# Kernel tuning notes

Hardware: AMD Instinct MI355X
Metric: run time of the kernel (lower is better)

The kernel has to match this reference:

```python
import jax, jax.numpy as jnp
import numpy as np

SEQ, BATCH, IN, H, HFC, OUT, NLAYERS = 1024, 64, 512, 1024, 512, 1, 2


def setup_inputs() -> dict:
    key = jax.random.key(0)
    ks = jax.random.split(key, 16)
    s_in = 1.0 / np.sqrt(H)  # torch RNN init scale: U(-1/sqrt(hidden), 1/sqrt(hidden))
    u = lambda k, shape: jax.random.uniform(k, shape, jnp.float32, -s_in, s_in)
    return {
        "x": jax.random.normal(ks[0], (SEQ, BATCH, IN), jnp.float32),
        "hidden": jnp.zeros((NLAYERS, BATCH, H), jnp.float32),
        # RNN layer 0
        "W_ih0": u(ks[1], (H, IN)),
        "W_hh0": u(ks[2], (H, H)),
        "b_ih0": u(ks[3], (H,)),
        "b_hh0": u(ks[4], (H,)),
        # RNN layer 1
        "W_ih1": u(ks[5], (H, H)),
        "W_hh1": u(ks[6], (H, H)),
        "b_ih1": u(ks[7], (H,)),
        "b_hh1": u(ks[8], (H,)),
        # FC head
        "W1": jax.random.normal(ks[9], (HFC, H), jnp.float32) / np.sqrt(H),
        "b1": jnp.zeros((HFC,), jnp.float32),
        "W2": jax.random.normal(ks[10], (OUT, HFC), jnp.float32) / np.sqrt(HFC),
        "b2": jnp.zeros((OUT,), jnp.float32),
    }


def _rnn_layer(inp, h0, W_ih, W_hh, b_ih, b_hh):
    # inp: (seq, batch, d_in); precompute input projection once (big GEMM)
    xW = jnp.einsum("sbi,hi->sbh", inp, W_ih) + b_ih + b_hh  # (seq, batch, H)

    def step(h, xw):
        h_new = jnp.tanh(xw + h @ W_hh.T)
        return h_new, h_new

    _, outs = jax.lax.scan(step, h0, xW)
    return outs  # (seq, batch, H)


def reference(x, hidden, W_ih0, W_hh0, b_ih0, b_hh0,
              W_ih1, W_hh1, b_ih1, b_hh1, W1, b1, W2, b2):
    r0 = _rnn_layer(x, hidden[0], W_ih0, W_hh0, b_ih0, b_hh0)
    r1 = _rnn_layer(r0, hidden[1], W_ih1, W_hh1, b_ih1, b_hh1)
    # Faithful to source: mean over dim=1, which (batch_first=False) is the batch dim
    pooled = jnp.mean(r1, axis=1)  # (seq, H)
    h1 = jax.nn.relu(pooled @ W1.T + b1)  # dropout is identity in eval mode
    out = jax.nn.sigmoid(h1 @ W2.T + b2)  # (seq, OUT)
    return out
```

## Files before the change

### kernel.cpp

```cpp
#include <hip/hip_runtime.h>

typedef unsigned int uint;
typedef unsigned short ushort;
typedef unsigned long long u64;
typedef __attribute__((ext_vector_type(8))) short s16x8;
typedef __attribute__((ext_vector_type(4))) float f32x4;
typedef __attribute__((ext_vector_type(4))) uint u32x4;

#define SEQ 1024
#define BATCH 64
#define INDIM 512
#define HID 1024

#define OFF_BUF   0ull
#define SZ_BUF    (65536ull * 1024ull * 2ull)
#define OFF_W0B   (OFF_BUF + SZ_BUF)
#define OFF_WH0B  (OFF_W0B  + 1048576ull)
#define OFF_W1B   (OFF_WH0B + 2097152ull)
#define OFF_WH1B  (OFF_W1B  + 2097152ull)
#define OFF_HINIT (OFF_WH1B + 2097152ull)
#define OFF_HDB1  (OFF_HINIT + 262144ull)
#define OFF_FLG   (OFF_HDB1 + 262144ull)
#define OFF_RING  (OFF_FLG + 131072ull)
#define OFF_PPART (OFF_RING + 4194304ull)
#define WS_NEEDED (OFF_PPART + 16777216ull)

__device__ __forceinline__ ushort f2bf(float f) {
    uint u = __float_as_uint(f);
    uint r = (u + 0x7fffu + ((u >> 16) & 1u)) >> 16;
    return (ushort)r;
}
__device__ __forceinline__ float bf2f(ushort h) {
    return __uint_as_float(((uint)h) << 16);
}

__device__ __forceinline__ void st16wt(void* p, uint v) {
    asm volatile("global_store_short %0, %1, off sc0 sc1"
                 :: "v"((u64)p), "v"(v) : "memory");
}
__device__ __forceinline__ void stf32wt(float* p, float v) {
    asm volatile("global_store_dword %0, %1, off sc0 sc1"
                 :: "v"((u64)p), "v"(v) : "memory");
}

__device__ __forceinline__ void poll_all(const uint* fp, uint tgt) {
    for (;;) {
        uint v = __hip_atomic_load(fp, __ATOMIC_RELAXED, __HIP_MEMORY_SCOPE_AGENT);
        if (__all(v >= tgt)) break;
        __builtin_amdgcn_s_sleep(1);
    }
}

__global__ void k_prep(const float* Wih0, const float* Whh0, const float* Wih1,
                       const float* Whh1, const float* hid, char* ws) {
    ushort* w0  = (ushort*)(ws + OFF_W0B);
    ushort* wh0 = (ushort*)(ws + OFF_WH0B);
    ushort* w1  = (ushort*)(ws + OFF_W1B);
    ushort* wh1 = (ushort*)(ws + OFF_WH1B);
    ushort* hi  = (ushort*)(ws + OFF_HINIT);
    uint*   flg = (uint*)(ws + OFF_FLG);
    const long long total = 524288 + 3 * 1048576 + 131072 + 32768;
    for (long long i = (long long)blockIdx.x * 256 + threadIdx.x; i < total;
         i += (long long)gridDim.x * 256) {
        long long j = i;
        if (j < 524288)  { w0[j]  = f2bf(Wih0[j]); continue; }  j -= 524288;
        if (j < 1048576) { wh0[j] = f2bf(Whh0[j]); continue; }  j -= 1048576;
        if (j < 1048576) { w1[j]  = f2bf(Wih1[j]); continue; }  j -= 1048576;
        if (j < 1048576) { wh1[j] = f2bf(Whh1[j]); continue; }  j -= 1048576;
        if (j < 131072)  { hi[j]  = f2bf(hid[j]);  continue; }  j -= 131072;
        flg[j] = 0u;
    }
}

__launch_bounds__(256)
__global__ void k_proj0(const float* __restrict__ x, const float* __restrict__ bih,
                        const float* __restrict__ bhh, char* ws) {
    const ushort* W = (const ushort*)(ws + OFF_W0B);
    ushort* cbuf = (ushort*)(ws + OFF_BUF);
    int bx = blockIdx.x;
    int mtile = bx >> 2, ntile = bx & 3;
    int tid = threadIdx.x, w = tid >> 6, l = tid & 63;
    int lr = l & 15, lq = l >> 4;
    int arow = mtile * 64 + w * 16 + lr;

    f32x4 acc[16];
#pragma unroll
    for (int i = 0; i < 16; i++) acc[i] = (f32x4){0.f, 0.f, 0.f, 0.f};

    for (int kc = 0; kc < 16; kc++) {
        int k0 = kc * 32 + lq * 8;
        const f32x4* ap = (const f32x4*)(x + (long long)arow * 512 + k0);
        f32x4 a0 = ap[0], a1 = ap[1];
        s16x8 a;
        a[0] = (short)f2bf(a0[0]); a[1] = (short)f2bf(a0[1]);
        a[2] = (short)f2bf(a0[2]); a[3] = (short)f2bf(a0[3]);
        a[4] = (short)f2bf(a1[0]); a[5] = (short)f2bf(a1[1]);
        a[6] = (short)f2bf(a1[2]); a[7] = (short)f2bf(a1[3]);
#pragma unroll
        for (int nf = 0; nf < 16; nf++) {
            int col = ntile * 256 + nf * 16 + lr;
            s16x8 b = *(const s16x8*)(W + (long long)col * 512 + k0);
            acc[nf] = __builtin_amdgcn_mfma_f32_16x16x32_bf16(a, b, acc[nf], 0, 0, 0);
        }
    }
#pragma unroll
    for (int nf = 0; nf < 16; nf++) {
        int col = ntile * 256 + nf * 16 + lr;
        float bb = bih[col] + bhh[col];
#pragma unroll
        for (int j = 0; j < 4; j++) {
            int row = mtile * 64 + w * 16 + lq * 4 + j;
            cbuf[(long long)row * 1024 + col] = f2bf(acc[nf][j] + bb);
        }
    }
}

__launch_bounds__(256, 1)
__global__ void k_recf(const ushort* __restrict__ wh0p, const ushort* __restrict__ wh1p,
                       const ushort* __restrict__ wxp,
                       ushort* __restrict__ cbuf, ushort* __restrict__ hdb1,
                       const ushort* __restrict__ hinitb, uint* __restrict__ flg,
                       float* __restrict__ ring, float* __restrict__ ppart,
                       const float* __restrict__ bih1, const float* __restrict__ bhh1) {
    int wgid = blockIdx.x;
    int x = wgid & 7, hi = wgid >> 3;
    int role, g, s;
    if (x < 4) { g = x; if (hi < 8) { role = 0; s = hi; } else { role = 2; s = hi - 8; } }
    else       { role = 1; g = x - 4; s = hi; }

    int tid = threadIdx.x;
    int l = tid & 63, wv = tid >> 6, lr = l & 15, lq = l >> 4;

    uint* f0g = flg + (g * 8) * 32;
    uint* f1g = flg + 1024 + (g * 8) * 32;
    uint* fcg = flg + 2048 + (g * 16) * 32;

    __shared__ __align__(16) char lds[32768];

    int colA = (role == 1) ? (s * 64 + wv * 16 + lr) : (s * 128 + wv * 16 + lr);
    int colB = (role == 1) ? colA : (s * 128 + 64 + wv * 16 + lr);
    const ushort* Wb = (role == 0) ? wh0p : (role == 1) ? wxp : wh1p;

    s16x8 wgtA[32], wgtB[32];
#pragma unroll
    for (int kc = 0; kc < 32; kc++)
        wgtA[kc] = *(const s16x8*)(Wb + (long long)colA * 1024 + kc * 32 + lq * 8);
#pragma unroll
    for (int kc = 0; kc < 32; kc++) asm volatile("" : "+v"(wgtA[kc]));
    if (role != 1) {
#pragma unroll
        for (int kc = 0; kc < 32; kc++)
            wgtB[kc] = *(const s16x8*)(Wb + (long long)colB * 1024 + kc * 32 + lq * 8);
#pragma unroll
        for (int kc = 0; kc < 32; kc++) asm volatile("" : "+v"(wgtB[kc]));
    }

    if (role == 1) {
        float bb = bih1[colA] + bhh1[colA];
        uint* myslot = fcg + s * 32;
        for (int k = 0; k < 128; k++) {
            if (tid < 64) {
                const uint* fp; uint tgt;
                int sl = l & 15;
                if (sl < 8) { fp = f0g + sl * 32; tgt = (uint)(8 * k + 8); }
                else        { fp = f1g + (sl - 8) * 32; tgt = (k >= 2) ? (uint)(8 * k - 8) : 0u; }
                poll_all(fp, tgt);
                if (l == 0)
                    (void)__hip_atomic_load(f0g, __ATOMIC_ACQUIRE, __HIP_MEMORY_SCOPE_AGENT);
            }
            __syncthreads();
            for (int tt = 0; tt < 8; tt++) {
                int t = 8 * k + tt;
                const char* src = (const char*)(cbuf + (t * 64 + g * 16) * 1024);
                u32x4 v[8];
#pragma unroll
                for (int i = 0; i < 8; i++)
                    v[i] = *(const u32x4*)(src + tid * 16 + i * 4096);
                __syncthreads();
#pragma unroll
                for (int i = 0; i < 8; i++) {
                    int off = tid * 16 + i * 4096;
                    int row = off >> 11;
                    int sw = (off & 2047) ^ ((row & 7) << 4);
                    *(u32x4*)(lds + row * 2048 + sw) = v[i];
                }
                __syncthreads();
                f32x4 a0c = (f32x4){0.f,0.f,0.f,0.f}, a1c = (f32x4){0.f,0.f,0.f,0.f};
#pragma unroll
                for (int kc = 0; kc < 32; kc += 2) {
                    int b0 = (kc * 64 + lq * 16) ^ ((lr & 7) << 4);
                    int b1 = ((kc + 1) * 64 + lq * 16) ^ ((lr & 7) << 4);
                    s16x8 fA = *(const s16x8*)(lds + lr * 2048 + b0);
                    s16x8 fB = *(const s16x8*)(lds + lr * 2048 + b1);
                    a0c = __builtin_amdgcn_mfma_f32_16x16x32_bf16(fA, wgtA[kc], a0c, 0, 0, 0);
                    a1c = __builtin_amdgcn_mfma_f32_16x16x32_bf16(fB, wgtA[kc + 1], a1c, 0, 0, 0);
                }
                float* rd = ring + (long long)((g * 16 + s) * 16 + (t & 15)) * 1024
                          + (wv * 16 + lr);
#pragma unroll
                for (int j = 0; j < 4; j++)
                    stf32wt(rd + (lq * 4 + j) * 64, a0c[j] + a1c[j] + bb);
            }
            __syncthreads();
            if (tid == 0)
                __hip_atomic_store(myslot, (uint)(8 * k + 8), __ATOMIC_RELEASE,
                                   __HIP_MEMORY_SCOPE_AGENT);
        }
        return;
    }

    uint* myslot = ((role == 0) ? f0g : f1g) + s * 32;
    const ushort* hinit = hinitb + (role == 2 ? 65536 : 0) + g * 16 * 1024;

    for (int t = 0; t < 1024; t++) {
        int cbase = (t * 64 + g * 16) * 1024;

        ushort cfA[4], cfB[4];
        if (role == 0) {
#pragma unroll
            for (int j = 0; j < 4; j++) {
                cfA[j] = cbuf[cbase + (lq * 4 + j) * 1024 + colA];
                cfB[j] = cbuf[cbase + (lq * 4 + j) * 1024 + colB];
            }
        }

        if (tid < 64) {
            if (role == 0) {
                poll_all(f0g + (l & 7) * 32, (uint)t);
            } else {
                const uint* fp; uint tgt;
                int sl = l & 15;
                if (sl < 8) { fp = f1g + sl * 32; tgt = (uint)t; }
                else if (sl < 10) { fp = fcg + (2 * s + (sl - 8)) * 32; tgt = (uint)(t + 1); }
                else { fp = f1g; tgt = (uint)t; }
                poll_all(fp, tgt);
            }
            if (l == 0)
                (void)__hip_atomic_load(f0g, __ATOMIC_ACQUIRE, __HIP_MEMORY_SCOPE_AGENT);
        }
        __syncthreads();

        float c1A[4], c1B[4];
        if (role == 2) {
            const float* rA = ring + (long long)((g * 16 + 2 * s) * 16 + (t & 15)) * 1024
                            + (wv * 16 + lr);
            const float* rB = ring + (long long)((g * 16 + 2 * s + 1) * 16 + (t & 15)) * 1024
                            + (wv * 16 + lr);
#pragma unroll
            for (int j = 0; j < 4; j++) {
                c1A[j] = rA[(lq * 4 + j) * 64];
                c1B[j] = rB[(lq * 4 + j) * 64];
            }
        }

        const char* src;
        if (role == 0)
            src = (const char*)((t == 0) ? hinit
                                         : (cbuf + ((t - 1) * 64 + g * 16) * 1024));
        else
            src = (const char*)((t == 0) ? hinit
                                         : (hdb1 + ((t - 1) & 1) * 65536 + g * 16 * 1024));
#pragma unroll
        for (int i = 0; i < 8; i++) {
            int off = tid * 16 + i * 4096;
            u32x4 v = *(const u32x4*)(src + off);
            int row = off >> 11;
            int sw = (off & 2047) ^ ((row & 7) << 4);
            *(u32x4*)(lds + row * 2048 + sw) = v;
        }
        __syncthreads();

        f32x4 aA0 = (f32x4){0.f,0.f,0.f,0.f}, aA1 = (f32x4){0.f,0.f,0.f,0.f};
        f32x4 aB0 = (f32x4){0.f,0.f,0.f,0.f}, aB1 = (f32x4){0.f,0.f,0.f,0.f};
#pragma unroll
        for (int kc = 0; kc < 32; kc += 2) {
            int b0 = (kc * 64 + lq * 16) ^ ((lr & 7) << 4);
            int b1 = ((kc + 1) * 64 + lq * 16) ^ ((lr & 7) << 4);
            s16x8 h0 = *(const s16x8*)(lds + lr * 2048 + b0);
            s16x8 h1 = *(const s16x8*)(lds + lr * 2048 + b1);
            aA0 = __builtin_amdgcn_mfma_f32_16x16x32_bf16(h0, wgtA[kc], aA0, 0, 0, 0);
            aB0 = __builtin_amdgcn_mfma_f32_16x16x32_bf16(h0, wgtB[kc], aB0, 0, 0, 0);
            aA1 = __builtin_amdgcn_mfma_f32_16x16x32_bf16(h1, wgtA[kc + 1], aA1, 0, 0, 0);
            aB1 = __builtin_amdgcn_mfma_f32_16x16x32_bf16(h1, wgtB[kc + 1], aB1, 0, 0, 0);
        }

        float hnA[4], hnB[4];
#pragma unroll
        for (int j = 0; j < 4; j++) {
            float zA = aA0[j] + aA1[j] + (role == 0 ? bf2f(cfA[j]) : c1A[j]);
            float zB = aB0[j] + aB1[j] + (role == 0 ? bf2f(cfB[j]) : c1B[j]);
            zA = fminf(fmaxf(zA, -15.f), 15.f);
            zB = fminf(fmaxf(zB, -15.f), 15.f);
            float eA = __expf(2.f * zA), eB = __expf(2.f * zB);
            hnA[j] = (eA - 1.f) / (eA + 1.f);
            hnB[j] = (eB - 1.f) / (eB + 1.f);
        }

        if (role == 0) {
#pragma unroll
            for (int j = 0; j < 4; j++) {
                st16wt(cbuf + cbase + (lq * 4 + j) * 1024 + colA, (uint)f2bf(hnA[j]));
                st16wt(cbuf + cbase + (lq * 4 + j) * 1024 + colB, (uint)f2bf(hnB[j]));
            }
        } else {
            ushort* hdst = hdb1 + (t & 1) * 65536 + g * 16 * 1024;
#pragma unroll
            for (int j = 0; j < 4; j++) {
                st16wt(hdst + (lq * 4 + j) * 1024 + colA, (uint)f2bf(hnA[j]));
                st16wt(hdst + (lq * 4 + j) * 1024 + colB, (uint)f2bf(hnB[j]));
            }
            float sA = hnA[0] + hnA[1] + hnA[2] + hnA[3];
            float sB = hnB[0] + hnB[1] + hnB[2] + hnB[3];
            sA += __shfl_xor(sA, 16); sA += __shfl_xor(sA, 32);
            sB += __shfl_xor(sB, 16); sB += __shfl_xor(sB, 32);
            if (l < 16) {
                stf32wt(&ppart[(g * 1024 + t) * 1024 + colA], sA);
                stf32wt(&ppart[(g * 1024 + t) * 1024 + colB], sB);
            }
        }

        __syncthreads();
        if (tid == 0)
            __hip_atomic_store(myslot, (uint)(t + 1), __ATOMIC_RELEASE,
                               __HIP_MEMORY_SCOPE_AGENT);
    }
}

__launch_bounds__(256)
__global__ void k_head(const float* __restrict__ W1, const float* __restrict__ b1,
                       const float* __restrict__ W2, const float* __restrict__ b2,
                       char* ws, float* __restrict__ out) {
    const float* pp = (const float*)(ws + OFF_PPART);
    int bx = blockIdx.x;
    int t0 = bx * 8;
    int tid = threadIdx.x;

    __shared__ float pl[8][1024];
    __shared__ float red[256][8];

    for (int i = tid; i < 8192; i += 256) {
        int tt = i >> 10, k = i & 1023;
        int base = (t0 + tt) * 1024 + k;
        float s = pp[base] + pp[1048576 + base] + pp[2097152 + base] + pp[3145728 + base];
        pl[tt][k] = s * (1.f / 64.f);
    }
    __syncthreads();

    float po[8];
#pragma unroll
    for (int tt = 0; tt < 8; tt++) po[tt] = 0.f;

    for (int jj = 0; jj < 2; jj++) {
        int j = tid + jj * 256;
        float accv[8];
        float bias = b1[j];
#pragma unroll
        for (int tt = 0; tt < 8; tt++) accv[tt] = bias;
        const float* wr = W1 + (long long)j * 1024;
        for (int k = 0; k < 1024; k += 8) {
            f32x4 wa = *(const f32x4*)(wr + k);
            f32x4 wb = *(const f32x4*)(wr + k + 4);
#pragma unroll
            for (int tt = 0; tt < 8; tt++) {
                accv[tt] += pl[tt][k] * wa[0] + pl[tt][k + 1] * wa[1] +
                            pl[tt][k + 2] * wa[2] + pl[tt][k + 3] * wa[3] +
                            pl[tt][k + 4] * wb[0] + pl[tt][k + 5] * wb[1] +
                            pl[tt][k + 6] * wb[2] + pl[tt][k + 7] * wb[3];
            }
        }
        float w2 = W2[j];
#pragma unroll
        for (int tt = 0; tt < 8; tt++) po[tt] += fmaxf(accv[tt], 0.f) * w2;
    }

#pragma unroll
    for (int tt = 0; tt < 8; tt++) red[tid][tt] = po[tt];
    __syncthreads();
    for (int st = 128; st >= 1; st >>= 1) {
        if (tid < st) {
#pragma unroll
            for (int tt = 0; tt < 8; tt++) red[tid][tt] += red[tid + st][tt];
        }
        __syncthreads();
    }
    if (tid < 8) out[t0 + tid] = 1.f / (1.f + __expf(-(red[0][tid] + b2[0])));
}

extern "C" void kernel_launch(void* const* d_in, const int* in_sizes, int n_in,
                              void* d_out, int out_size, void* d_ws, size_t ws_size,
                              hipStream_t stream) {
    const float* x    = (const float*)d_in[0];
    const float* hid  = (const float*)d_in[1];
    const float* Wih0 = (const float*)d_in[2];
    const float* Whh0 = (const float*)d_in[3];
    const float* bih0 = (const float*)d_in[4];
    const float* bhh0 = (const float*)d_in[5];
    const float* Wih1 = (const float*)d_in[6];
    const float* Whh1 = (const float*)d_in[7];
    const float* bih1 = (const float*)d_in[8];
    const float* bhh1 = (const float*)d_in[9];
    const float* W1   = (const float*)d_in[10];
    const float* b1   = (const float*)d_in[11];
    const float* W2   = (const float*)d_in[12];
    const float* b2   = (const float*)d_in[13];
    char* ws = (char*)d_ws;
    float* out = (float*)d_out;

    hipLaunchKernelGGL(k_prep, dim3(1024), dim3(256), 0, stream,
                       Wih0, Whh0, Wih1, Whh1, hid, ws);
    hipLaunchKernelGGL(k_proj0, dim3(4096), dim3(256), 0, stream, x, bih0, bhh0, ws);
    hipLaunchKernelGGL(k_recf, dim3(128), dim3(256), 0, stream,
                       (const ushort*)(ws + OFF_WH0B), (const ushort*)(ws + OFF_WH1B),
                       (const ushort*)(ws + OFF_W1B),
                       (ushort*)(ws + OFF_BUF), (ushort*)(ws + OFF_HDB1),
                       (const ushort*)(ws + OFF_HINIT), (uint*)(ws + OFF_FLG),
                       (float*)(ws + OFF_RING), (float*)(ws + OFF_PPART),
                       bih1, bhh1);
    hipLaunchKernelGGL(k_head, dim3(128), dim3(256), 0, stream, W1, b1, W2, b2, ws, out);
}
```

Baseline: 6.574 ms.

## Repartition recurrent kernel into two batch groups of 32 rows across 48 workgroups

The persistent recurrent kernel now splits the batch into 2 groups of 32 rows instead of 4 groups of 16, and each workgroup runs two M-tiles per step. The layer-1 input-projection role now covers 128 columns like the recurrent roles, so the grid drops from 128 to 48 workgroups. The aim is fewer workgroups and fewer flags to synchronise, more MFMA work per weight register load, and a cheaper head reduction over 2 partial sums instead of 4. In exchange each step does twice the per-workgroup compute and LDS traffic, with a 64KB LDS buffer, which may lengthen the serial critical path of each timestep.

```diff
diff --git a/kernel.cpp b/kernel.cpp
--- a/kernel.cpp
+++ b/kernel.cpp
@@ -23,7 +23,7 @@
 #define OFF_FLG   (OFF_HDB1 + 262144ull)
 #define OFF_RING  (OFF_FLG + 131072ull)
 #define OFF_PPART (OFF_RING + 4194304ull)
-#define WS_NEEDED (OFF_PPART + 16777216ull)
+#define WS_NEEDED (OFF_PPART + 8388608ull)
 
 __device__ __forceinline__ ushort f2bf(float f) {
     uint u = __float_as_uint(f);
@@ -123,22 +123,22 @@
                        float* __restrict__ ring, float* __restrict__ ppart,
                        const float* __restrict__ bih1, const float* __restrict__ bhh1) {
     int wgid = blockIdx.x;
-    int x = wgid & 7, hi = wgid >> 3;
-    int role, g, s;
-    if (x < 4) { g = x; if (hi < 8) { role = 0; s = hi; } else { role = 2; s = hi - 8; } }
-    else       { role = 1; g = x - 4; s = hi; }
+    int x = wgid & 7, h = wgid >> 3;
+    int g = x >> 2;
+    int idx = (x & 3) * 6 + h;
+    int role = idx >> 3, s = idx & 7;
 
     int tid = threadIdx.x;
     int l = tid & 63, wv = tid >> 6, lr = l & 15, lq = l >> 4;
 
     uint* f0g = flg + (g * 8) * 32;
     uint* f1g = flg + 1024 + (g * 8) * 32;
-    uint* fcg = flg + 2048 + (g * 16) * 32;
-
-    __shared__ __align__(16) char lds[32768];
-
-    int colA = (role == 1) ? (s * 64 + wv * 16 + lr) : (s * 128 + wv * 16 + lr);
-    int colB = (role == 1) ? colA : (s * 128 + 64 + wv * 16 + lr);
+    uint* fcg = flg + 2048 + (g * 8) * 32;
+
+    __shared__ __align__(16) char lds[65536];
+
+    int colA = s * 128 + wv * 16 + lr;
+    int colB = colA + 64;
     const ushort* Wb = (role == 0) ? wh0p : (role == 1) ? wxp : wh1p;
 
     s16x8 wgtA[32], wgtB[32];
@@ -147,16 +147,34 @@
         wgtA[kc] = *(const s16x8*)(Wb + (long long)colA * 1024 + kc * 32 + lq * 8);
 #pragma unroll
     for (int kc = 0; kc < 32; kc++) asm volatile("" : "+v"(wgtA[kc]));
-    if (role != 1) {
-#pragma unroll
-        for (int kc = 0; kc < 32; kc++)
-            wgtB[kc] = *(const s16x8*)(Wb + (long long)colB * 1024 + kc * 32 + lq * 8);
-#pragma unroll
-        for (int kc = 0; kc < 32; kc++) asm volatile("" : "+v"(wgtB[kc]));
+#pragma unroll
+    for (int kc = 0; kc < 32; kc++)
+        wgtB[kc] = *(const s16x8*)(Wb + (long long)colB * 1024 + kc * 32 + lq * 8);
+#pragma unroll
+    for (int kc = 0; kc < 32; kc++) asm volatile("" : "+v"(wgtB[kc]));
+
+#define STWR(i, val) { int off = tid * 16 + (i) * 4096; int row = off >> 11;        \
+                       int sw = (off & 2047) ^ ((row & 7) << 4);                    \
+                       *(u32x4*)(lds + row * 2048 + sw) = (val); }
+#define GEMM32(accA, accB)                                                          \
+    _Pragma("unroll")                                                               \
+    for (int kc = 0; kc < 32; kc += 2) {                                            \
+        int b0 = (kc * 64 + lq * 16) ^ ((lr & 7) << 4);                             \
+        int b1 = ((kc + 1) * 64 + lq * 16) ^ ((lr & 7) << 4);                       \
+        _Pragma("unroll")                                                           \
+        for (int m = 0; m < 2; m++) {                                               \
+            s16x8 h0 = *(const s16x8*)(lds + (m * 16 + lr) * 2048 + b0);            \
+            s16x8 h1 = *(const s16x8*)(lds + (m * 16 + lr) * 2048 + b1);            \
+            accA[m][0] = __builtin_amdgcn_mfma_f32_16x16x32_bf16(h0, wgtA[kc], accA[m][0], 0, 0, 0); \
+            accB[m][0] = __builtin_amdgcn_mfma_f32_16x16x32_bf16(h0, wgtB[kc], accB[m][0], 0, 0, 0); \
+            accA[m][1] = __builtin_amdgcn_mfma_f32_16x16x32_bf16(h1, wgtA[kc + 1], accA[m][1], 0, 0, 0); \
+            accB[m][1] = __builtin_amdgcn_mfma_f32_16x16x32_bf16(h1, wgtB[kc + 1], accB[m][1], 0, 0, 0); \
+        }                                                                           \
     }
 
     if (role == 1) {
-        float bb = bih1[colA] + bhh1[colA];
+        float bbA = bih1[colA] + bhh1[colA];
+        float bbB = bih1[colB] + bhh1[colB];
         uint* myslot = fcg + s * 32;
         for (int k = 0; k < 128; k++) {
             if (tid < 64) {
@@ -171,35 +189,35 @@
             __syncthreads();
             for (int tt = 0; tt < 8; tt++) {
                 int t = 8 * k + tt;
-                const char* src = (const char*)(cbuf + (t * 64 + g * 16) * 1024);
-                u32x4 v[8];
-#pragma unroll
-                for (int i = 0; i < 8; i++)
+                const char* src = (const char*)(cbuf + (t * 64 + g * 32) * 1024);
+                u32x4 v[16];
+#pragma unroll
+                for (int i = 0; i < 16; i++)
                     v[i] = *(const u32x4*)(src + tid * 16 + i * 4096);
                 __syncthreads();
 #pragma unroll
-                for (int i = 0; i < 8; i++) {
-                    int off = tid * 16 + i * 4096;
-                    int row = off >> 11;
-                    int sw = (off & 2047) ^ ((row & 7) << 4);
-                    *(u32x4*)(lds + row * 2048 + sw) = v[i];
-                }
+                for (int i = 0; i < 16; i++) STWR(i, v[i])
                 __syncthreads();
-                f32x4 a0c = (f32x4){0.f,0.f,0.f,0.f}, a1c = (f32x4){0.f,0.f,0.f,0.f};
-#pragma unroll
-                for (int kc = 0; kc < 32; kc += 2) {
-                    int b0 = (kc * 64 + lq * 16) ^ ((lr & 7) << 4);
-                    int b1 = ((kc + 1) * 64 + lq * 16) ^ ((lr & 7) << 4);
-                    s16x8 fA = *(const s16x8*)(lds + lr * 2048 + b0);
-                    s16x8 fB = *(const s16x8*)(lds + lr * 2048 + b1);
-                    a0c = __builtin_amdgcn_mfma_f32_16x16x32_bf16(fA, wgtA[kc], a0c, 0, 0, 0);
-                    a1c = __builtin_amdgcn_mfma_f32_16x16x32_bf16(fB, wgtA[kc + 1], a1c, 0, 0, 0);
-                }
-                float* rd = ring + (long long)((g * 16 + s) * 16 + (t & 15)) * 1024
+                f32x4 accA[2][2], accB[2][2];
+#pragma unroll
+                for (int m = 0; m < 2; m++)
+#pragma unroll
+                    for (int u = 0; u < 2; u++) {
+                        accA[m][u] = (f32x4){0.f, 0.f, 0.f, 0.f};
+                        accB[m][u] = (f32x4){0.f, 0.f, 0.f, 0.f};
+                    }
+                GEMM32(accA, accB)
+                float* rd = ring + (long long)((g * 8 + s) * 16 + (t & 15)) * 4096
                           + (wv * 16 + lr);
 #pragma unroll
-                for (int j = 0; j < 4; j++)
-                    stf32wt(rd + (lq * 4 + j) * 64, a0c[j] + a1c[j] + bb);
+                for (int m = 0; m < 2; m++)
+#pragma unroll
+                    for (int j = 0; j < 4; j++) {
+                        stf32wt(rd + (m * 16 + lq * 4 + j) * 128,
+                                accA[m][0][j] + accA[m][1][j] + bbA);
+                        stf32wt(rd + (m * 16 + lq * 4 + j) * 128 + 64,
+                                accB[m][0][j] + accB[m][1][j] + bbB);
+                    }
             }
             __syncthreads();
             if (tid == 0)
@@ -210,18 +228,20 @@
     }
 
     uint* myslot = ((role == 0) ? f0g : f1g) + s * 32;
-    const ushort* hinit = hinitb + (role == 2 ? 65536 : 0) + g * 16 * 1024;
+    const ushort* hinit = hinitb + (role == 2 ? 65536 : 0) + g * 32 * 1024;
 
     for (int t = 0; t < 1024; t++) {
-        int cbase = (t * 64 + g * 16) * 1024;
-
-        ushort cfA[4], cfB[4];
+        int cbase = (t * 64 + g * 32) * 1024;
+
+        ushort cfA[2][4], cfB[2][4];
         if (role == 0) {
 #pragma unroll
-            for (int j = 0; j < 4; j++) {
-                cfA[j] = cbuf[cbase + (lq * 4 + j) * 1024 + colA];
-                cfB[j] = cbuf[cbase + (lq * 4 + j) * 1024 + colB];
-            }
+            for (int m = 0; m < 2; m++)
+#pragma unroll
+                for (int j = 0; j < 4; j++) {
+                    cfA[m][j] = cbuf[cbase + (m * 16 + lq * 4 + j) * 1024 + colA];
+                    cfB[m][j] = cbuf[cbase + (m * 16 + lq * 4 + j) * 1024 + colB];
+                }
         }
 
         if (tid < 64) {
@@ -229,10 +249,9 @@
                 poll_all(f0g + (l & 7) * 32, (uint)t);
             } else {
                 const uint* fp; uint tgt;
-                int sl = l & 15;
-                if (sl < 8) { fp = f1g + sl * 32; tgt = (uint)t; }
-                else if (sl < 10) { fp = fcg + (2 * s + (sl - 8)) * 32; tgt = (uint)(t + 1); }
-                else { fp = f1g; tgt = (uint)t; }
+                if (l < 8)       { fp = f1g + l * 32; tgt = (uint)t; }
+                else if (l == 8) { fp = fcg + s * 32; tgt = (uint)(t + 1); }
+                else             { fp = f1g; tgt = (uint)t; }
                 poll_all(fp, tgt);
             }
             if (l == 0)
@@ -240,77 +259,84 @@
         }
         __syncthreads();
 
-        float c1A[4], c1B[4];
+        float c1A[2][4], c1B[2][4];
         if (role == 2) {
-            const float* rA = ring + (long long)((g * 16 + 2 * s) * 16 + (t & 15)) * 1024
+            const float* rs = ring + (long long)((g * 8 + s) * 16 + (t & 15)) * 4096
                             + (wv * 16 + lr);
-            const float* rB = ring + (long long)((g * 16 + 2 * s + 1) * 16 + (t & 15)) * 1024
-                            + (wv * 16 + lr);
-#pragma unroll
-            for (int j = 0; j < 4; j++) {
-                c1A[j] = rA[(lq * 4 + j) * 64];
-                c1B[j] = rB[(lq * 4 + j) * 64];
-            }
+#pragma unroll
+            for (int m = 0; m < 2; m++)
+#pragma unroll
+                for (int j = 0; j < 4; j++) {
+                    c1A[m][j] = rs[(m * 16 + lq * 4 + j) * 128];
+                    c1B[m][j] = rs[(m * 16 + lq * 4 + j) * 128 + 64];
+                }
         }
 
         const char* src;
         if (role == 0)
             src = (const char*)((t == 0) ? hinit
-                                         : (cbuf + ((t - 1) * 64 + g * 16) * 1024));
+                                         : (cbuf + ((t - 1) * 64 + g * 32) * 1024));
         else
             src = (const char*)((t == 0) ? hinit
-                                         : (hdb1 + ((t - 1) & 1) * 65536 + g * 16 * 1024));
-#pragma unroll
-        for (int i = 0; i < 8; i++) {
-            int off = tid * 16 + i * 4096;
-            u32x4 v = *(const u32x4*)(src + off);
-            int row = off >> 11;
-            int sw = (off & 2047) ^ ((row & 7) << 4);
-            *(u32x4*)(lds + row * 2048 + sw) = v;
+                                         : (hdb1 + ((t - 1) & 1) * 65536 + g * 32 * 1024));
+#pragma unroll
+        for (int i = 0; i < 16; i++) {
+            u32x4 v = *(const u32x4*)(src + tid * 16 + i * 4096);
+            STWR(i, v)
         }
         __syncthreads();
 
-        f32x4 aA0 = (f32x4){0.f,0.f,0.f,0.f}, aA1 = (f32x4){0.f,0.f,0.f,0.f};
-        f32x4 aB0 = (f32x4){0.f,0.f,0.f,0.f}, aB1 = (f32x4){0.f,0.f,0.f,0.f};
-#pragma unroll
-        for (int kc = 0; kc < 32; kc += 2) {
-            int b0 = (kc * 64 + lq * 16) ^ ((lr & 7) << 4);
-            int b1 = ((kc + 1) * 64 + lq * 16) ^ ((lr & 7) << 4);
-            s16x8 h0 = *(const s16x8*)(lds + lr * 2048 + b0);
-            s16x8 h1 = *(const s16x8*)(lds + lr * 2048 + b1);
-            aA0 = __builtin_amdgcn_mfma_f32_16x16x32_bf16(h0, wgtA[kc], aA0, 0, 0, 0);
-            aB0 = __builtin_amdgcn_mfma_f32_16x16x32_bf16(h0, wgtB[kc], aB0, 0, 0, 0);
-            aA1 = __builtin_amdgcn_mfma_f32_16x16x32_bf16(h1, wgtA[kc + 1], aA1, 0, 0, 0);
-            aB1 = __builtin_amdgcn_mfma_f32_16x16x32_bf16(h1, wgtB[kc + 1], aB1, 0, 0, 0);
-        }
-
-        float hnA[4], hnB[4];
-#pragma unroll
-        for (int j = 0; j < 4; j++) {
-            float zA = aA0[j] + aA1[j] + (role == 0 ? bf2f(cfA[j]) : c1A[j]);
-            float zB = aB0[j] + aB1[j] + (role == 0 ? bf2f(cfB[j]) : c1B[j]);
-            zA = fminf(fmaxf(zA, -15.f), 15.f);
-            zB = fminf(fmaxf(zB, -15.f), 15.f);
-            float eA = __expf(2.f * zA), eB = __expf(2.f * zB);
-            hnA[j] = (eA - 1.f) / (eA + 1.f);
-            hnB[j] = (eB - 1.f) / (eB + 1.f);
-        }
+        f32x4 accA[2][2], accB[2][2];
+#pragma unroll
+        for (int m = 0; m < 2; m++)
+#pragma unroll
+            for (int u = 0; u < 2; u++) {
+                accA[m][u] = (f32x4){0.f, 0.f, 0.f, 0.f};
+                accB[m][u] = (f32x4){0.f, 0.f, 0.f, 0.f};
+            }
+        GEMM32(accA, accB)
+
+        float hnA[2][4], hnB[2][4];
+#pragma unroll
+        for (int m = 0; m < 2; m++)
+#pragma unroll
+            for (int j = 0; j < 4; j++) {
+                float zA = accA[m][0][j] + accA[m][1][j]
+                         + (role == 0 ? bf2f(cfA[m][j]) : c1A[m][j]);
+                float zB = accB[m][0][j] + accB[m][1][j]
+                         + (role == 0 ? bf2f(cfB[m][j]) : c1B[m][j]);
+                zA = fminf(fmaxf(zA, -15.f), 15.f);
+                zB = fminf(fmaxf(zB, -15.f), 15.f);
+                float eA = __expf(2.f * zA), eB = __expf(2.f * zB);
+                hnA[m][j] = (eA - 1.f) / (eA + 1.f);
+                hnB[m][j] = (eB - 1.f) / (eB + 1.f);
+            }
 
         if (role == 0) {
 #pragma unroll
-            for (int j = 0; j < 4; j++) {
-                st16wt(cbuf + cbase + (lq * 4 + j) * 1024 + colA, (uint)f2bf(hnA[j]));
-                st16wt(cbuf + cbase + (lq * 4 + j) * 1024 + colB, (uint)f2bf(hnB[j]));
-            }
+            for (int m = 0; m < 2; m++)
+#pragma unroll
+                for (int j = 0; j < 4; j++) {
+                    st16wt(cbuf + cbase + (m * 16 + lq * 4 + j) * 1024 + colA,
+                           (uint)f2bf(hnA[m][j]));
+                    st16wt(cbuf + cbase + (m * 16 + lq * 4 + j) * 1024 + colB,
+                           (uint)f2bf(hnB[m][j]));
+                }
         } else {
-            ushort* hdst = hdb1 + (t & 1) * 65536 + g * 16 * 1024;
-#pragma unroll
-            for (int j = 0; j < 4; j++) {
-                st16wt(hdst + (lq * 4 + j) * 1024 + colA, (uint)f2bf(hnA[j]));
-                st16wt(hdst + (lq * 4 + j) * 1024 + colB, (uint)f2bf(hnB[j]));
-            }
-            float sA = hnA[0] + hnA[1] + hnA[2] + hnA[3];
-            float sB = hnB[0] + hnB[1] + hnB[2] + hnB[3];
+            ushort* hdst = hdb1 + (t & 1) * 65536 + g * 32 * 1024;
+#pragma unroll
+            for (int m = 0; m < 2; m++)
+#pragma unroll
+                for (int j = 0; j < 4; j++) {
+                    st16wt(hdst + (m * 16 + lq * 4 + j) * 1024 + colA,
+                           (uint)f2bf(hnA[m][j]));
+                    st16wt(hdst + (m * 16 + lq * 4 + j) * 1024 + colB,
+                           (uint)f2bf(hnB[m][j]));
+                }
+            float sA = hnA[0][0] + hnA[0][1] + hnA[0][2] + hnA[0][3]
+                     + hnA[1][0] + hnA[1][1] + hnA[1][2] + hnA[1][3];
+            float sB = hnB[0][0] + hnB[0][1] + hnB[0][2] + hnB[0][3]
+                     + hnB[1][0] + hnB[1][1] + hnB[1][2] + hnB[1][3];
             sA += __shfl_xor(sA, 16); sA += __shfl_xor(sA, 32);
             sB += __shfl_xor(sB, 16); sB += __shfl_xor(sB, 32);
             if (l < 16) {
@@ -324,6 +350,8 @@
             __hip_atomic_store(myslot, (uint)(t + 1), __ATOMIC_RELEASE,
                                __HIP_MEMORY_SCOPE_AGENT);
     }
+#undef GEMM32
+#undef STWR
 }
 
 __launch_bounds__(256)
@@ -341,7 +369,7 @@
     for (int i = tid; i < 8192; i += 256) {
         int tt = i >> 10, k = i & 1023;
         int base = (t0 + tt) * 1024 + k;
-        float s = pp[base] + pp[1048576 + base] + pp[2097152 + base] + pp[3145728 + base];
+        float s = pp[base] + pp[1048576 + base];
         pl[tt][k] = s * (1.f / 64.f);
     }
     __syncthreads();
@@ -409,7 +437,7 @@
     hipLaunchKernelGGL(k_prep, dim3(1024), dim3(256), 0, stream,
                        Wih0, Whh0, Wih1, Whh1, hid, ws);
     hipLaunchKernelGGL(k_proj0, dim3(4096), dim3(256), 0, stream, x, bih0, bhh0, ws);
-    hipLaunchKernelGGL(k_recf, dim3(128), dim3(256), 0, stream,
+    hipLaunchKernelGGL(k_recf, dim3(48), dim3(256), 0, stream,
                        (const ushort*)(ws + OFF_WH0B), (const ushort*)(ws + OFF_WH1B),
                        (const ushort*)(ws + OFF_W1B),
                        (ushort*)(ws + OFF_BUF), (ushort*)(ws + OFF_HDB1),
```

New measurement: 9.938 ms. 51.2% more time.

## Fuse layer-1 input projection into layer-1 recurrence workgroups, drop ring buffer

Applied to the files above, without the earlier changes.

Removes the separate role that computed layer-1 input projections in 8-step chunks into a float ring buffer. Each layer-1 workgroup now owns 64 columns and holds both W_hh1 and W_ih1 slices in registers, computing h@W_hh and x@W_ih per step from two LDS tiles. This cuts the extra flag handshake and ring round-trip through global memory and reduces the grid from 128 to 96 workgroups. The cost is twice the MFMA work and staging per step on the layer-1 critical path, and a shorter lookahead for layer 1 behind layer 0.

```diff
diff --git a/kernel.cpp b/kernel.cpp
--- a/kernel.cpp
+++ b/kernel.cpp
@@ -21,8 +21,7 @@
 #define OFF_HINIT (OFF_WH1B + 2097152ull)
 #define OFF_HDB1  (OFF_HINIT + 262144ull)
 #define OFF_FLG   (OFF_HDB1 + 262144ull)
-#define OFF_RING  (OFF_FLG + 131072ull)
-#define OFF_PPART (OFF_RING + 4194304ull)
+#define OFF_PPART (OFF_FLG + 131072ull)
 #define WS_NEEDED (OFF_PPART + 16777216ull)
 
 __device__ __forceinline__ ushort f2bf(float f) {
@@ -120,210 +119,193 @@
                        const ushort* __restrict__ wxp,
                        ushort* __restrict__ cbuf, ushort* __restrict__ hdb1,
                        const ushort* __restrict__ hinitb, uint* __restrict__ flg,
-                       float* __restrict__ ring, float* __restrict__ ppart,
+                       float* __restrict__ ppart,
                        const float* __restrict__ bih1, const float* __restrict__ bhh1) {
     int wgid = blockIdx.x;
-    int x = wgid & 7, hi = wgid >> 3;
-    int role, g, s;
-    if (x < 4) { g = x; if (hi < 8) { role = 0; s = hi; } else { role = 2; s = hi - 8; } }
-    else       { role = 1; g = x - 4; s = hi; }
+    int g = wgid & 3;
+    int r = wgid >> 2;
+    int role = (r < 8) ? 0 : 1;
+    int s = (r < 8) ? r : (r - 8);
 
     int tid = threadIdx.x;
     int l = tid & 63, wv = tid >> 6, lr = l & 15, lq = l >> 4;
 
     uint* f0g = flg + (g * 8) * 32;
-    uint* f1g = flg + 1024 + (g * 8) * 32;
-    uint* fcg = flg + 2048 + (g * 16) * 32;
-
-    __shared__ __align__(16) char lds[32768];
-
-    int colA = (role == 1) ? (s * 64 + wv * 16 + lr) : (s * 128 + wv * 16 + lr);
-    int colB = (role == 1) ? colA : (s * 128 + 64 + wv * 16 + lr);
-    const ushort* Wb = (role == 0) ? wh0p : (role == 1) ? wxp : wh1p;
-
-    s16x8 wgtA[32], wgtB[32];
-#pragma unroll
-    for (int kc = 0; kc < 32; kc++)
-        wgtA[kc] = *(const s16x8*)(Wb + (long long)colA * 1024 + kc * 32 + lq * 8);
-#pragma unroll
-    for (int kc = 0; kc < 32; kc++) asm volatile("" : "+v"(wgtA[kc]));
-    if (role != 1) {
+    uint* f1g = flg + 1024 + (g * 16) * 32;
+
+    __shared__ __align__(16) char lds[65536];
+    char* ldsH = lds;
+    char* ldsX = lds + 32768;
+
+#define STWRB(base, i, val) { int off = tid * 16 + (i) * 4096; int row = off >> 11;  \
+                              int sw = (off & 2047) ^ ((row & 7) << 4);              \
+                              *(u32x4*)((base) + row * 2048 + sw) = (val); }
+
+    if (role == 0) {
+        int colA = s * 128 + wv * 16 + lr;
+        int colB = colA + 64;
+        s16x8 wgtA[32], wgtB[32];
 #pragma unroll
         for (int kc = 0; kc < 32; kc++)
-            wgtB[kc] = *(const s16x8*)(Wb + (long long)colB * 1024 + kc * 32 + lq * 8);
+            wgtA[kc] = *(const s16x8*)(wh0p + (long long)colA * 1024 + kc * 32 + lq * 8);
+#pragma unroll
+        for (int kc = 0; kc < 32; kc++) asm volatile("" : "+v"(wgtA[kc]));
+#pragma unroll
+        for (int kc = 0; kc < 32; kc++)
+            wgtB[kc] = *(const s16x8*)(wh0p + (long long)colB * 1024 + kc * 32 + lq * 8);
 #pragma unroll
         for (int kc = 0; kc < 32; kc++) asm volatile("" : "+v"(wgtB[kc]));
-    }
-
-    if (role == 1) {
-        float bb = bih1[colA] + bhh1[colA];
-        uint* myslot = fcg + s * 32;
-        for (int k = 0; k < 128; k++) {
-            if (tid < 64) {
-                const uint* fp; uint tgt;
-                int sl = l & 15;
-                if (sl < 8) { fp = f0g + sl * 32; tgt = (uint)(8 * k + 8); }
-                else        { fp = f1g + (sl - 8) * 32; tgt = (k >= 2) ? (uint)(8 * k - 8) : 0u; }
-                poll_all(fp, tgt);
-                if (l == 0)
-                    (void)__hip_atomic_load(f0g, __ATOMIC_ACQUIRE, __HIP_MEMORY_SCOPE_AGENT);
-            }
-            __syncthreads();
-            for (int tt = 0; tt < 8; tt++) {
-                int t = 8 * k + tt;
-                const char* src = (const char*)(cbuf + (t * 64 + g * 16) * 1024);
-                u32x4 v[8];
-#pragma unroll
-                for (int i = 0; i < 8; i++)
-                    v[i] = *(const u32x4*)(src + tid * 16 + i * 4096);
-                __syncthreads();
-#pragma unroll
-                for (int i = 0; i < 8; i++) {
-                    int off = tid * 16 + i * 4096;
-                    int row = off >> 11;
-                    int sw = (off & 2047) ^ ((row & 7) << 4);
-                    *(u32x4*)(lds + row * 2048 + sw) = v[i];
-                }
-                __syncthreads();
-                f32x4 a0c = (f32x4){0.f,0.f,0.f,0.f}, a1c = (f32x4){0.f,0.f,0.f,0.f};
-#pragma unroll
-                for (int kc = 0; kc < 32; kc += 2) {
-                    int b0 = (kc * 64 + lq * 16) ^ ((lr & 7) << 4);
-                    int b1 = ((kc + 1) * 64 + lq * 16) ^ ((lr & 7) << 4);
-                    s16x8 fA = *(const s16x8*)(lds + lr * 2048 + b0);
-                    s16x8 fB = *(const s16x8*)(lds + lr * 2048 + b1);
-                    a0c = __builtin_amdgcn_mfma_f32_16x16x32_bf16(fA, wgtA[kc], a0c, 0, 0, 0);
-                    a1c = __builtin_amdgcn_mfma_f32_16x16x32_bf16(fB, wgtA[kc + 1], a1c, 0, 0, 0);
-                }
-                float* rd = ring + (long long)((g * 16 + s) * 16 + (t & 15)) * 1024
-                          + (wv * 16 + lr);
-#pragma unroll
-                for (int j = 0; j < 4; j++)
-                    stf32wt(rd + (lq * 4 + j) * 64, a0c[j] + a1c[j] + bb);
-            }
-            __syncthreads();
-            if (tid == 0)
-                __hip_atomic_store(myslot, (uint)(8 * k + 8), __ATOMIC_RELEASE,
-                                   __HIP_MEMORY_SCOPE_AGENT);
-        }
-        return;
-    }
-
-    uint* myslot = ((role == 0) ? f0g : f1g) + s * 32;
-    const ushort* hinit = hinitb + (role == 2 ? 65536 : 0) + g * 16 * 1024;
-
-    for (int t = 0; t < 1024; t++) {
-        int cbase = (t * 64 + g * 16) * 1024;
-
-        ushort cfA[4], cfB[4];
-        if (role == 0) {
+
+        uint* myslot = f0g + s * 32;
+        const ushort* hinit = hinitb + g * 16 * 1024;
+
+        for (int t = 0; t < 1024; t++) {
+            int cbase = (t * 64 + g * 16) * 1024;
+
+            ushort cfA[4], cfB[4];
 #pragma unroll
             for (int j = 0; j < 4; j++) {
                 cfA[j] = cbuf[cbase + (lq * 4 + j) * 1024 + colA];
                 cfB[j] = cbuf[cbase + (lq * 4 + j) * 1024 + colB];
             }
-        }
+
+            if (tid < 64) {
+                poll_all(f0g + (l & 7) * 32, (uint)t);
+                if (l == 0)
+                    (void)__hip_atomic_load(f0g, __ATOMIC_ACQUIRE, __HIP_MEMORY_SCOPE_AGENT);
+            }
+            __syncthreads();
+
+            const char* src = (const char*)((t == 0) ? hinit
+                                : (cbuf + ((t - 1) * 64 + g * 16) * 1024));
+#pragma unroll
+            for (int i = 0; i < 8; i++) {
+                u32x4 v = *(const u32x4*)(src + tid * 16 + i * 4096);
+                STWRB(ldsH, i, v)
+            }
+            __syncthreads();
+
+            f32x4 aA0 = (f32x4){0.f,0.f,0.f,0.f}, aA1 = (f32x4){0.f,0.f,0.f,0.f};
+            f32x4 aB0 = (f32x4){0.f,0.f,0.f,0.f}, aB1 = (f32x4){0.f,0.f,0.f,0.f};
+#pragma unroll
+            for (int kc = 0; kc < 32; kc += 2) {
+                int b0 = (kc * 64 + lq * 16) ^ ((lr & 7) << 4);
+                int b1 = ((kc + 1) * 64 + lq * 16) ^ ((lr & 7) << 4);
+                s16x8 h0 = *(const s16x8*)(ldsH + lr * 2048 + b0);
+                s16x8 h1 = *(const s16x8*)(ldsH + lr * 2048 + b1);
+                aA0 = __builtin_amdgcn_mfma_f32_16x16x32_bf16(h0, wgtA[kc], aA0, 0, 0, 0);
+                aB0 = __builtin_amdgcn_mfma_f32_16x16x32_bf16(h0, wgtB[kc], aB0, 0, 0, 0);
+                aA1 = __builtin_amdgcn_mfma_f32_16x16x32_bf16(h1, wgtA[kc + 1], aA1, 0, 0, 0);
+                aB1 = __builtin_amdgcn_mfma_f32_16x16x32_bf16(h1, wgtB[kc + 1], aB1, 0, 0, 0);
+            }
+
+#pragma unroll
+            for (int j = 0; j < 4; j++) {
+                float zA = aA0[j] + aA1[j] + bf2f(cfA[j]);
+                float zB = aB0[j] + aB1[j] + bf2f(cfB[j]);
+                zA = fminf(fmaxf(zA, -15.f), 15.f);
+                zB = fminf(fmaxf(zB, -15.f), 15.f);
+                float eA = __expf(2.f * zA), eB = __expf(2.f * zB);
+                float hA = (eA - 1.f) / (eA + 1.f);
+                float hB = (eB - 1.f) / (eB + 1.f);
+                st16wt(cbuf + cbase + (lq * 4 + j) * 1024 + colA, (uint)f2bf(hA));
+                st16wt(cbuf + cbase + (lq * 4 + j) * 1024 + colB, (uint)f2bf(hB));
+            }
+
+            __syncthreads();
+            if (tid == 0)
+                __hip_atomic_store(myslot, (uint)(t + 1), __ATOMIC_RELEASE,
+                                   __HIP_MEMORY_SCOPE_AGENT);
+        }
+        return;
+    }
+
+    int col = s * 64 + wv * 16 + lr;
+    s16x8 wgt[32], wxt[32];
+#pragma unroll
+    for (int kc = 0; kc < 32; kc++)
+        wgt[kc] = *(const s16x8*)(wh1p + (long long)col * 1024 + kc * 32 + lq * 8);
+#pragma unroll
+    for (int kc = 0; kc < 32; kc++) asm volatile("" : "+v"(wgt[kc]));
+#pragma unroll
+    for (int kc = 0; kc < 32; kc++)
+        wxt[kc] = *(const s16x8*)(wxp + (long long)col * 1024 + kc * 32 + lq * 8);
+#pragma unroll
+    for (int kc = 0; kc < 32; kc++) asm volatile("" : "+v"(wxt[kc]));
+
+    float bb = bih1[col] + bhh1[col];
+    uint* myslot = f1g + s * 32;
+    const ushort* hinit = hinitb + 65536 + g * 16 * 1024;
+
+    for (int t = 0; t < 1024; t++) {
+        int cbase = (t * 64 + g * 16) * 1024;
 
         if (tid < 64) {
-            if (role == 0) {
-                poll_all(f0g + (l & 7) * 32, (uint)t);
-            } else {
-                const uint* fp; uint tgt;
-                int sl = l & 15;
-                if (sl < 8) { fp = f1g + sl * 32; tgt = (uint)t; }
-                else if (sl < 10) { fp = fcg + (2 * s + (sl - 8)) * 32; tgt = (uint)(t + 1); }
-                else { fp = f1g; tgt = (uint)t; }
-                poll_all(fp, tgt);
-            }
+            const uint* fp; uint tgt;
+            if (l < 8)       { fp = f0g + l * 32; tgt = (uint)(t + 1); }
+            else if (l < 24) { fp = f1g + (l - 8) * 32; tgt = (uint)t; }
+            else             { fp = f0g; tgt = 0u; }
+            poll_all(fp, tgt);
             if (l == 0)
                 (void)__hip_atomic_load(f0g, __ATOMIC_ACQUIRE, __HIP_MEMORY_SCOPE_AGENT);
         }
         __syncthreads();
 
-        float c1A[4], c1B[4];
-        if (role == 2) {
-            const float* rA = ring + (long long)((g * 16 + 2 * s) * 16 + (t & 15)) * 1024
-                            + (wv * 16 + lr);
-            const float* rB = ring + (long long)((g * 16 + 2 * s + 1) * 16 + (t & 15)) * 1024
-                            + (wv * 16 + lr);
-#pragma unroll
-            for (int j = 0; j < 4; j++) {
-                c1A[j] = rA[(lq * 4 + j) * 64];
-                c1B[j] = rB[(lq * 4 + j) * 64];
-            }
-        }
-
-        const char* src;
-        if (role == 0)
-            src = (const char*)((t == 0) ? hinit
-                                         : (cbuf + ((t - 1) * 64 + g * 16) * 1024));
-        else
-            src = (const char*)((t == 0) ? hinit
-                                         : (hdb1 + ((t - 1) & 1) * 65536 + g * 16 * 1024));
+        const char* xsrc = (const char*)(cbuf + cbase);
 #pragma unroll
         for (int i = 0; i < 8; i++) {
-            int off = tid * 16 + i * 4096;
-            u32x4 v = *(const u32x4*)(src + off);
-            int row = off >> 11;
-            int sw = (off & 2047) ^ ((row & 7) << 4);
-            *(u32x4*)(lds + row * 2048 + sw) = v;
+            u32x4 v = *(const u32x4*)(xsrc + tid * 16 + i * 4096);
+            STWRB(ldsX, i, v)
+        }
+        const char* hsrc = (const char*)((t == 0) ? hinit
+                            : (hdb1 + ((t - 1) & 1) * 65536 + g * 16 * 1024));
+#pragma unroll
+        for (int i = 0; i < 8; i++) {
+            u32x4 v = *(const u32x4*)(hsrc + tid * 16 + i * 4096);
+            STWRB(ldsH, i, v)
         }
         __syncthreads();
 
-        f32x4 aA0 = (f32x4){0.f,0.f,0.f,0.f}, aA1 = (f32x4){0.f,0.f,0.f,0.f};
-        f32x4 aB0 = (f32x4){0.f,0.f,0.f,0.f}, aB1 = (f32x4){0.f,0.f,0.f,0.f};
+        f32x4 ah0 = (f32x4){0.f,0.f,0.f,0.f}, ah1 = (f32x4){0.f,0.f,0.f,0.f};
+        f32x4 ax0 = (f32x4){0.f,0.f,0.f,0.f}, ax1 = (f32x4){0.f,0.f,0.f,0.f};
 #pragma unroll
         for (int kc = 0; kc < 32; kc += 2) {
             int b0 = (kc * 64 + lq * 16) ^ ((lr & 7) << 4);
             int b1 = ((kc + 1) * 64 + lq * 16) ^ ((lr & 7) << 4);
-            s16x8 h0 = *(const s16x8*)(lds + lr * 2048 + b0);
-            s16x8 h1 = *(const s16x8*)(lds + lr * 2048 + b1);
-            aA0 = __builtin_amdgcn_mfma_f32_16x16x32_bf16(h0, wgtA[kc], aA0, 0, 0, 0);
-            aB0 = __builtin_amdgcn_mfma_f32_16x16x32_bf16(h0, wgtB[kc], aB0, 0, 0, 0);
-            aA1 = __builtin_amdgcn_mfma_f32_16x16x32_bf16(h1, wgtA[kc + 1], aA1, 0, 0, 0);
-            aB1 = __builtin_amdgcn_mfma_f32_16x16x32_bf16(h1, wgtB[kc + 1], aB1, 0, 0, 0);
-        }
-
-        float hnA[4], hnB[4];
+            s16x8 h0 = *(const s16x8*)(ldsH + lr * 2048 + b0);
+            s16x8 h1 = *(const s16x8*)(ldsH + lr * 2048 + b1);
+            s16x8 x0 = *(const s16x8*)(ldsX + lr * 2048 + b0);
+            s16x8 x1 = *(const s16x8*)(ldsX + lr * 2048 + b1);
+            ah0 = __builtin_amdgcn_mfma_f32_16x16x32_bf16(h0, wgt[kc], ah0, 0, 0, 0);
+            ax0 = __builtin_amdgcn_mfma_f32_16x16x32_bf16(x0, wxt[kc], ax0, 0, 0, 0);
+            ah1 = __builtin_amdgcn_mfma_f32_16x16x32_bf16(h1, wgt[kc + 1], ah1, 0, 0, 0);
+            ax1 = __builtin_amdgcn_mfma_f32_16x16x32_bf16(x1, wxt[kc + 1], ax1, 0, 0, 0);
+        }
+
+        float hn[4];
 #pragma unroll
         for (int j = 0; j < 4; j++) {
-            float zA = aA0[j] + aA1[j] + (role == 0 ? bf2f(cfA[j]) : c1A[j]);
-            float zB = aB0[j] + aB1[j] + (role == 0 ? bf2f(cfB[j]) : c1B[j]);
-            zA = fminf(fmaxf(zA, -15.f), 15.f);
-            zB = fminf(fmaxf(zB, -15.f), 15.f);
-            float eA = __expf(2.f * zA), eB = __expf(2.f * zB);
-            hnA[j] = (eA - 1.f) / (eA + 1.f);
-            hnB[j] = (eB - 1.f) / (eB + 1.f);
-        }
-
-        if (role == 0) {
-#pragma unroll
-            for (int j = 0; j < 4; j++) {
-                st16wt(cbuf + cbase + (lq * 4 + j) * 1024 + colA, (uint)f2bf(hnA[j]));
-                st16wt(cbuf + cbase + (lq * 4 + j) * 1024 + colB, (uint)f2bf(hnB[j]));
-            }
-        } else {
-            ushort* hdst = hdb1 + (t & 1) * 65536 + g * 16 * 1024;
-#pragma unroll
-            for (int j = 0; j < 4; j++) {
-                st16wt(hdst + (lq * 4 + j) * 1024 + colA, (uint)f2bf(hnA[j]));
-                st16wt(hdst + (lq * 4 + j) * 1024 + colB, (uint)f2bf(hnB[j]));
-            }
-            float sA = hnA[0] + hnA[1] + hnA[2] + hnA[3];
-            float sB = hnB[0] + hnB[1] + hnB[2] + hnB[3];
-            sA += __shfl_xor(sA, 16); sA += __shfl_xor(sA, 32);
-            sB += __shfl_xor(sB, 16); sB += __shfl_xor(sB, 32);
-            if (l < 16) {
-                stf32wt(&ppart[(g * 1024 + t) * 1024 + colA], sA);
-                stf32wt(&ppart[(g * 1024 + t) * 1024 + colB], sB);
-            }
-        }
+            float z = ah0[j] + ah1[j] + ax0[j] + ax1[j] + bb;
+            z = fminf(fmaxf(z, -15.f), 15.f);
+            float e = __expf(2.f * z);
+            hn[j] = (e - 1.f) / (e + 1.f);
+        }
+
+        ushort* hdst = hdb1 + (t & 1) * 65536 + g * 16 * 1024;
+#pragma unroll
+        for (int j = 0; j < 4; j++)
+            st16wt(hdst + (lq * 4 + j) * 1024 + col, (uint)f2bf(hn[j]));
+        float sm = hn[0] + hn[1] + hn[2] + hn[3];
+        sm += __shfl_xor(sm, 16);
+        sm += __shfl_xor(sm, 32);
+        if (l < 16) stf32wt(&ppart[(g * 1024 + t) * 1024 + col], sm);
 
         __syncthreads();
         if (tid == 0)
             __hip_atomic_store(myslot, (uint)(t + 1), __ATOMIC_RELEASE,
                                __HIP_MEMORY_SCOPE_AGENT);
     }
+#undef STWRB
 }
 
 __launch_bounds__(256)
@@ -409,12 +391,11 @@
     hipLaunchKernelGGL(k_prep, dim3(1024), dim3(256), 0, stream,
                        Wih0, Whh0, Wih1, Whh1, hid, ws);
     hipLaunchKernelGGL(k_proj0, dim3(4096), dim3(256), 0, stream, x, bih0, bhh0, ws);
-    hipLaunchKernelGGL(k_recf, dim3(128), dim3(256), 0, stream,
+    hipLaunchKernelGGL(k_recf, dim3(96), dim3(256), 0, stream,
                        (const ushort*)(ws + OFF_WH0B), (const ushort*)(ws + OFF_WH1B),
                        (const ushort*)(ws + OFF_W1B),
                        (ushort*)(ws + OFF_BUF), (ushort*)(ws + OFF_HDB1),
                        (const ushort*)(ws + OFF_HINIT), (uint*)(ws + OFF_FLG),
-                       (float*)(ws + OFF_RING), (float*)(ws + OFF_PPART),
-                       bih1, bhh1);
+                       (float*)(ws + OFF_PPART), bih1, bhh1);
     hipLaunchKernelGGL(k_head, dim3(128), dim3(256), 0, stream, W1, b1, W2, b2, ws, out);
 }
```

New measurement: 8.444 ms. +28.5%, slower.
